# Performance work log

Measured on AMD Instinct MI355X. Metric: run time of the kernel, lower is better.

## Reference

```python
import jax, jax.numpy as jnp
import numpy as np

EMBED_DIM = 1024
NUM_HEADS = 16
HEAD_DIM = EMBED_DIM // NUM_HEADS


def setup_inputs() -> dict:
    key = jax.random.key(0)
    ks = jax.random.split(key, 5)
    B, T, C = 2, 2048, EMBED_DIM
    s_in = 1.0 / np.sqrt(C)
    x = jax.random.normal(ks[0], (B, T, C), dtype=jnp.float32)
    W_qkv = jax.random.normal(ks[1], (C, 3 * C), dtype=jnp.float32) * s_in
    b_qkv = jnp.zeros((3 * C,), dtype=jnp.float32)
    W_out = jax.random.normal(ks[2], (C, C), dtype=jnp.float32) * s_in
    b_out = jnp.zeros((C,), dtype=jnp.float32)
    return {"x": x, "W_qkv": W_qkv, "b_qkv": b_qkv, "W_out": W_out, "b_out": b_out}


def reference(x, W_qkv, b_qkv, W_out, b_out):
    B, T, C = x.shape
    H, D = NUM_HEADS, HEAD_DIM
    qkv = x @ W_qkv + b_qkv                      # [B,T,3C]
    qkv = qkv.reshape(B, T, 3, H, D)
    q = jnp.transpose(qkv[:, :, 0], (0, 2, 1, 3))  # [B,H,T,D]
    k = jnp.transpose(qkv[:, :, 1], (0, 2, 1, 3))
    v = jnp.transpose(qkv[:, :, 2], (0, 2, 1, 3))
    scores = jnp.einsum('bhtd,bhsd->bhts', q, k) / np.sqrt(D).astype(jnp.float32)
    attn = jax.nn.softmax(scores, axis=-1)
    ctx = jnp.einsum('bhts,bhsd->bhtd', attn, v)   # [B,H,T,D]
    ctx = jnp.transpose(ctx, (0, 2, 1, 3)).reshape(B, T, C)
    return ctx @ W_out + b_out
```

## Files before the change

kernel.cpp:

```cpp
#include <hip/hip_runtime.h>
#include <hip/hip_bf16.h>


typedef __attribute__((ext_vector_type(8)))  short short8;
typedef __attribute__((ext_vector_type(4)))  float floatx4;
typedef __attribute__((ext_vector_type(16))) float floatx16;

__device__ inline ushort f2bf(float f) {
    union { __hip_bfloat16 h; ushort u; } c; c.h = __float2bfloat16(f); return c.u;
}

__device__ inline uint cvt_pk_bf16(float a, float b) {
    uint r;
    asm("v_cvt_pk_bf16_f32 %0, %1, %2" : "=v"(r) : "v"(a), "v"(b));
    return r;
}

__device__ inline void gld16(const ushort* g, ushort* l) {
    __builtin_amdgcn_global_load_lds(
        (__attribute__((address_space(1))) void*)(g),
        (__attribute__((address_space(3))) void*)(l), 16, 0, 0);
}

__device__ inline void tile_transpose(const float* __restrict__ src, ushort* __restrict__ dst,
                                      int R, int C, int rt, int ct, int t, ushort* L)
{
    const int row = t >> 2, cc = (t & 3) * 16;
    const float* sp = src + (long)(rt * 64 + row) * C + ct * 64 + cc;
    ushort tmp[16];
    #pragma unroll
    for (int i = 0; i < 4; i++) {
        float4 v = *(const float4*)(sp + i * 4);
        tmp[i*4+0]=f2bf(v.x); tmp[i*4+1]=f2bf(v.y); tmp[i*4+2]=f2bf(v.z); tmp[i*4+3]=f2bf(v.w);
    }
    *(uint4*)&L[row * 72 + cc]     = *(uint4*)&tmp[0];
    *(uint4*)&L[row * 72 + cc + 8] = *(uint4*)&tmp[8];
    __syncthreads();
    const int c = t >> 2, rc = (t & 3) * 16;
    ushort o[16];
    #pragma unroll
    for (int j = 0; j < 16; j++) o[j] = L[(rc + j) * 72 + c];
    ushort* dp = dst + (long)(ct * 64 + c) * R + rt * 64 + rc;
    *(uint4*)dp       = *(uint4*)&o[0];
    *(uint4*)(dp + 8) = *(uint4*)&o[8];
}

__global__ __launch_bounds__(256) void prep_kernel(
    const float* __restrict__ x, const float* __restrict__ Wqkv, const float* __restrict__ Wout,
    ushort* __restrict__ xb, ushort* __restrict__ wqkvT, ushort* __restrict__ woutT)
{
    __shared__ __align__(16) ushort L[64 * 72];
    const int bid = blockIdx.x, t = threadIdx.x;
    if (bid < 2048) {
        long i = ((long)bid * 256 + t) * 8;
        float4 a = *(const float4*)(x + i);
        float4 b = *(const float4*)(x + i + 4);
        ushort tmp[8] = { f2bf(a.x), f2bf(a.y), f2bf(a.z), f2bf(a.w),
                          f2bf(b.x), f2bf(b.y), f2bf(b.z), f2bf(b.w) };
        *(uint4*)(xb + i) = *(uint4*)tmp;
    } else if (bid < 2048 + 768) {
        int idx = bid - 2048;
        tile_transpose(Wqkv, wqkvT, 1024, 3072, idx & 15, idx >> 4, t, L);
    } else {
        int idx = bid - 2048 - 768;
        tile_transpose(Wout, woutT, 1024, 1024, idx & 15, idx >> 4, t, L);
    }
}

#define QSCALE 0.18033688011112042f

__global__ __launch_bounds__(256, 3) void qkv_gemm_kernel(
    const ushort* __restrict__ A, const ushort* __restrict__ Bt,
    const float* __restrict__ bias,
    ushort* __restrict__ qbuf, ushort* __restrict__ kbuf, ushort* __restrict__ vtG)
{
    __shared__ __align__(16) ushort SMEM[16384];
    ushort* Asb[2] = { SMEM,        SMEM + 4096 };
    ushort* Bsb[2] = { SMEM + 8192, SMEM + 12288 };

    const int t = threadIdx.x;
    const int w = t >> 6, lane = t & 63;
    const int r = lane & 15, qq = lane >> 4;
    const int wm = w >> 1, wn = w & 1;

    const int id = blockIdx.x;
    const int xcd = id & 7, cidx = id >> 3;
    const int lx = cidx % 12, ly = cidx / 12;
    const int bx = (xcd & 1) * 12 + lx;
    const int by = (xcd >> 1) * 8 + ly;
    const int rowBase = by * 128, colBase = bx * 128;

    const int g_row = lane >> 2, g_kc = (lane & 3) * 8;
    const ushort* aP0 = A  + (long)(rowBase +      w * 16 + g_row) * 1024 + g_kc;
    const ushort* aP1 = A  + (long)(rowBase + 64 + w * 16 + g_row) * 1024 + g_kc;
    const ushort* bP0 = Bt + (long)(colBase +      w * 16 + g_row) * 1024 + g_kc;
    const ushort* bP1 = Bt + (long)(colBase + 64 + w * 16 + g_row) * 1024 + g_kc;

    floatx4 acc[4][4] = {};

    for (int k0 = 0; k0 < 1024; k0 += 64) {
        #pragma unroll
        for (int kk = 0; kk < 2; kk++) {
            gld16(aP0 + k0 + kk * 32, &Asb[kk][(w * 16) * 32]);
            gld16(aP1 + k0 + kk * 32, &Asb[kk][(64 + w * 16) * 32]);
            gld16(bP0 + k0 + kk * 32, &Bsb[kk][(w * 16) * 32]);
            gld16(bP1 + k0 + kk * 32, &Bsb[kk][(64 + w * 16) * 32]);
        }
        __syncthreads();
        #pragma unroll
        for (int kk = 0; kk < 2; kk++) {
            short8 af[4], bf4[4];
            #pragma unroll
            for (int tm = 0; tm < 4; tm++) af[tm]  = *(const short8*)&Asb[kk][(wm * 64 + tm * 16 + r) * 32 + qq * 8];
            #pragma unroll
            for (int tn = 0; tn < 4; tn++) bf4[tn] = *(const short8*)&Bsb[kk][(wn * 64 + tn * 16 + r) * 32 + qq * 8];
            #pragma unroll
            for (int tm = 0; tm < 4; tm++)
                #pragma unroll
                for (int tn = 0; tn < 4; tn++)
                    acc[tm][tn] = __builtin_amdgcn_mfma_f32_16x16x32_bf16(af[tm], bf4[tn], acc[tm][tn], 0, 0, 0);
        }
        __syncthreads();
    }

    if (colBase < 2048) {
        #pragma unroll
        for (int tn = 0; tn < 4; tn++) {
            int col = colBase + wn * 64 + tn * 16 + r;
            float bvv = bias[col];
            #pragma unroll
            for (int tm = 0; tm < 4; tm++) {
                #pragma unroll
                for (int reg = 0; reg < 4; reg++) {
                    int row = rowBase + wm * 64 + tm * 16 + qq * 4 + reg;
                    float val = acc[tm][tn][reg] + bvv;
                    if (colBase < 1024) qbuf[(long)row * 1024 + col]        = f2bf(val * QSCALE);
                    else                kbuf[(long)row * 1024 + col - 1024] = f2bf(val);
                }
            }
        }
    } else {
        ushort* L = SMEM;
        #pragma unroll
        for (int hh = 0; hh < 2; hh++) {
            __syncthreads();
            if (wn == hh) {
                #pragma unroll
                for (int tn = 0; tn < 4; tn++) {
                    int vc = tn * 16 + r;
                    float bvv = bias[colBase + wn * 64 + vc];
                    #pragma unroll
                    for (int tm = 0; tm < 4; tm++) {
                        int row0 = wm * 64 + tm * 16 + qq * 4;
                        ushort q4[4] = { f2bf(acc[tm][tn][0] + bvv), f2bf(acc[tm][tn][1] + bvv),
                                         f2bf(acc[tm][tn][2] + bvv), f2bf(acc[tm][tn][3] + bvv) };
                        *(uint2*)&L[vc * 136 + row0] = *(uint2*)q4;
                    }
                }
            }
            __syncthreads();
            int d = t >> 2, tq = (t & 3) * 32;
            int h_loc = ((colBase - 2048) >> 6) + hh;
            long vtrow = (long)((rowBase >> 11) * 16 + h_loc) * 64 + d;
            ushort* dst = vtG + vtrow * 2048 + (rowBase & 2047) + tq;
            #pragma unroll
            for (int i = 0; i < 4; i++)
                *(uint4*)(dst + 8 * i) = *(uint4*)&L[d * 136 + tq + 8 * i];
        }
    }
}

__global__ __launch_bounds__(256) void out_gemm_kernel(
    const ushort* __restrict__ A, const ushort* __restrict__ Bt,
    const float* __restrict__ bias, float* __restrict__ out)
{
    __shared__ __align__(16) ushort As[2][128 * 32];
    __shared__ __align__(16) ushort Bs[2][64 * 32];

    const int t = threadIdx.x;
    const int w = t >> 6, lane = t & 63;
    const int r = lane & 15, qq = lane >> 4;
    const int wm = w >> 1, wn = w & 1;

    const int id = blockIdx.x;
    const int xcd = id & 7, cidx = id >> 3;
    const int bx = (xcd & 1) * 8 + (cidx & 7);
    const int by = (xcd >> 1) * 8 + (cidx >> 3);
    const int rowBase = by * 128, colBase = bx * 64;

    const int g_row = lane >> 2, g_kc = (lane & 3) * 8;
    const ushort* aP0 = A  + (long)(rowBase +      w * 16 + g_row) * 1024 + g_kc;
    const ushort* aP1 = A  + (long)(rowBase + 64 + w * 16 + g_row) * 1024 + g_kc;
    const ushort* bP0 = Bt + (long)(colBase +      w * 16 + g_row) * 1024 + g_kc;

    floatx4 acc[4][2] = {};

    for (int k0 = 0; k0 < 1024; k0 += 64) {
        #pragma unroll
        for (int kk = 0; kk < 2; kk++) {
            gld16(aP0 + k0 + kk * 32, &As[kk][(w * 16) * 32]);
            gld16(aP1 + k0 + kk * 32, &As[kk][(64 + w * 16) * 32]);
            gld16(bP0 + k0 + kk * 32, &Bs[kk][(w * 16) * 32]);
        }
        __syncthreads();
        #pragma unroll
        for (int kk = 0; kk < 2; kk++) {
            short8 af[4], bf2[2];
            #pragma unroll
            for (int tm = 0; tm < 4; tm++) af[tm]  = *(const short8*)&As[kk][(wm * 64 + tm * 16 + r) * 32 + qq * 8];
            #pragma unroll
            for (int tn = 0; tn < 2; tn++) bf2[tn] = *(const short8*)&Bs[kk][(wn * 32 + tn * 16 + r) * 32 + qq * 8];
            #pragma unroll
            for (int tm = 0; tm < 4; tm++)
                #pragma unroll
                for (int tn = 0; tn < 2; tn++)
                    acc[tm][tn] = __builtin_amdgcn_mfma_f32_16x16x32_bf16(af[tm], bf2[tn], acc[tm][tn], 0, 0, 0);
        }
        __syncthreads();
    }

    #pragma unroll
    for (int tn = 0; tn < 2; tn++) {
        int col = colBase + wn * 32 + tn * 16 + r;
        float bvv = bias[col];
        #pragma unroll
        for (int tm = 0; tm < 4; tm++) {
            #pragma unroll
            for (int reg = 0; reg < 4; reg++) {
                int row = rowBase + wm * 64 + tm * 16 + qq * 4 + reg;
                out[(long)row * 1024 + col] = acc[tm][tn][reg] + bvv;
            }
        }
    }
}

__global__ __launch_bounds__(512, 4) void attn_kernel(
    ushort* __restrict__ qbuf, const ushort* __restrict__ kbuf,
    const ushort* __restrict__ vt)
{
    __shared__ __align__(16) ushort SM[2][2][2][64 * 72];

    const int t = threadIdx.x;
    const int w = t >> 6, lane = t & 63;
    const int m32 = lane & 31, hi = lane >> 5;
    const int h2 = w >> 2, wq = w & 3;

    const int id = blockIdx.x;
    const int j = id >> 3;
    const int bh = (id & 7) * 4 + (j >> 4);
    const int qt = j & 15;
    const int b = bh >> 4, h = bh & 15;
    const long qrow = (long)(b * 2048 + qt * 128 + wq * 32 + m32);

    short8 qfrag[4];
    #pragma unroll
    for (int dc = 0; dc < 4; dc++)
        qfrag[dc] = *(const short8*)(qbuf + qrow * 1024 + h * 64 + dc * 16 + hi * 8);

    short8 vones;
    #pragma unroll
    for (int i = 0; i < 8; i++) vones[i] = (short)0x3F80;

    const int ts = t & 255;
    const int srow = ts >> 2, scol = (ts & 3) * 16;
    const ushort* kP = kbuf + (long)(b * 2048 + h2 * 1024 + srow) * 1024 + h * 64 + scol;
    const ushort* vP = vt + (long)(bh * 64 + srow) * 2048 + h2 * 1024 + scol;

    floatx16 o[2] = {};
    floatx16 lacc = {};

    uint4 kr0, kr1, vr0, vr1;

    kr0 = *(const uint4*)kP;  kr1 = *(const uint4*)(kP + 8);
    vr0 = *(const uint4*)vP;  vr1 = *(const uint4*)(vP + 8);
    {
        ushort* Ks = SM[h2][0][0]; ushort* Vs = SM[h2][0][1];
        *(uint4*)&Ks[srow * 72 + scol]     = kr0;
        *(uint4*)&Ks[srow * 72 + scol + 8] = kr1;
        *(uint4*)&Vs[srow * 72 + scol]     = vr0;
        *(uint4*)&Vs[srow * 72 + scol + 8] = vr1;
    }
    kr0 = *(const uint4*)(kP + 64 * 1024); kr1 = *(const uint4*)(kP + 64 * 1024 + 8);
    vr0 = *(const uint4*)(vP + 64);        vr1 = *(const uint4*)(vP + 64 + 8);
    __syncthreads();

    #pragma unroll 2
    for (int tt = 0; tt < 16; tt++) {
        ushort* Ks = SM[h2][tt & 1][0];
        ushort* Vs = SM[h2][tt & 1][1];

        floatx16 s[2] = {};
        __builtin_amdgcn_s_setprio(1);
        #pragma unroll
        for (int c = 0; c < 2; c++) {
            #pragma unroll
            for (int dc = 0; dc < 4; dc++) {
                short8 kf = *(const short8*)&Ks[(c * 32 + m32) * 72 + dc * 16 + hi * 8];
                s[c] = __builtin_amdgcn_mfma_f32_32x32x16_bf16(kf, qfrag[dc], s[c], 0, 0, 0);
            }
        }
        __builtin_amdgcn_s_setprio(0);

        if (tt < 15) {
            ushort* Kn = SM[h2][(tt + 1) & 1][0];
            ushort* Vn = SM[h2][(tt + 1) & 1][1];
            *(uint4*)&Kn[srow * 72 + scol]     = kr0;
            *(uint4*)&Kn[srow * 72 + scol + 8] = kr1;
            *(uint4*)&Vn[srow * 72 + scol]     = vr0;
            *(uint4*)&Vn[srow * 72 + scol + 8] = vr1;
            if (tt < 14) {
                const ushort* kp = kP + (long)(tt + 2) * 64 * 1024;
                const ushort* vp = vP + (tt + 2) * 64;
                kr0 = *(const uint4*)kp; kr1 = *(const uint4*)(kp + 8);
                vr0 = *(const uint4*)vp; vr1 = *(const uint4*)(vp + 8);
            }
        }

        uint pk[2][8];
        #pragma unroll
        for (int c = 0; c < 2; c++) {
            #pragma unroll
            for (int i = 0; i < 8; i++) {
                float p0 = __builtin_amdgcn_exp2f(s[c][2 * i]);
                float p1 = __builtin_amdgcn_exp2f(s[c][2 * i + 1]);
                pk[c][i] = cvt_pk_bf16(p0, p1);
            }
        }

        __builtin_amdgcn_s_setprio(1);
        #pragma unroll
        for (int c = 0; c < 2; c++) {
            #pragma unroll
            for (int kc = 0; kc < 2; kc++) {
                uint a0 = pk[c][4 * kc + 0], b0 = pk[c][4 * kc + 2];
                asm("v_permlane32_swap_b32 %0, %1" : "+v"(a0), "+v"(b0));
                uint a1 = pk[c][4 * kc + 1], b1 = pk[c][4 * kc + 3];
                asm("v_permlane32_swap_b32 %0, %1" : "+v"(a1), "+v"(b1));
                union { uint u[4]; short8 s8; } cv;
                cv.u[0] = a0; cv.u[1] = a1; cv.u[2] = b0; cv.u[3] = b1;
                #pragma unroll
                for (int dt = 0; dt < 2; dt++) {
                    short8 vf = *(const short8*)&Vs[(dt * 32 + m32) * 72 + c * 32 + kc * 16 + hi * 8];
                    o[dt] = __builtin_amdgcn_mfma_f32_32x32x16_bf16(vf, cv.s8, o[dt], 0, 0, 0);
                }
                lacc = __builtin_amdgcn_mfma_f32_32x32x16_bf16(vones, cv.s8, lacc, 0, 0, 0);
            }
        }
        __builtin_amdgcn_s_setprio(0);

        __syncthreads();
    }

    float* OL = (float*)SM;
    float* LL = OL + 4 * 2048;
    if (h2 == 1) {
        #pragma unroll
        for (int dt = 0; dt < 2; dt++)
            #pragma unroll
            for (int i = 0; i < 16; i++)
                OL[wq * 2048 + (dt * 16 + i) * 64 + lane] = o[dt][i];
        LL[wq * 64 + lane] = lacc[0];
    }
    __syncthreads();
    if (h2 == 0) {
        float inv = 1.f / (lacc[0] + LL[wq * 64 + lane]);
        #pragma unroll
        for (int dt = 0; dt < 2; dt++) {
            #pragma unroll
            for (int i = 0; i < 16; i++) o[dt][i] += OL[wq * 2048 + (dt * 16 + i) * 64 + lane];
            #pragma unroll
            for (int g = 0; g < 4; g++) {
                ushort tmp[4] = { f2bf(o[dt][4*g+0] * inv), f2bf(o[dt][4*g+1] * inv),
                                  f2bf(o[dt][4*g+2] * inv), f2bf(o[dt][4*g+3] * inv) };
                *(uint2*)(qbuf + qrow * 1024 + h * 64 + dt * 32 + g * 8 + hi * 4) = *(uint2*)tmp;
            }
        }
    }
}

extern "C" void kernel_launch(void* const* d_in, const int* in_sizes, int n_in,
                              void* d_out, int out_size, void* d_ws, size_t ws_size,
                              hipStream_t stream) {
    const float* x     = (const float*)d_in[0];
    const float* W_qkv = (const float*)d_in[1];
    const float* b_qkv = (const float*)d_in[2];
    const float* W_out = (const float*)d_in[3];
    const float* b_out = (const float*)d_in[4];
    float* out = (float*)d_out;

    ushort* qbuf  = (ushort*)d_ws;
    ushort* kbuf  = qbuf + (size_t)4096 * 1024;
    ushort* vt    = kbuf + (size_t)4096 * 1024;
    ushort* woutT = vt + (size_t)2048 * 2048;
    ushort* wqkvT = woutT + (size_t)1024 * 1024;

    ushort* xb    = (ushort*)d_out;

    dim3 blk(256);
    prep_kernel<<<3072, blk, 0, stream>>>(x, W_qkv, W_out, xb, wqkvT, woutT);
    qkv_gemm_kernel<<<768, blk, 0, stream>>>(xb, wqkvT, b_qkv, qbuf, kbuf, vt);
    attn_kernel<<<512, dim3(512), 0, stream>>>(qbuf, kbuf, vt);
    out_gemm_kernel<<<512, blk, 0, stream>>>(qbuf, woutT, b_out, out);
}
```

Measured before the change: 186.8 us.

## Double-buffer LDS in QKV and output GEMMs to overlap loads with MFMA

Both projection GEMMs switch from a load-all-then-compute loop over 64-wide K steps to a ping-pong double buffer over 32-wide K steps. The next tile's global-to-LDS loads are issued before the current tile's MFMAs, and only one barrier is used per step. The goal is to hide global load latency behind matrix math. The cost is twice as many loop iterations and barriers, and it relies on the single barrier being enough to keep the buffers correctly ordered.

```diff
diff --git a/kernel.cpp b/kernel.cpp
--- a/kernel.cpp
+++ b/kernel.cpp
@@ -75,8 +75,6 @@
     ushort* __restrict__ qbuf, ushort* __restrict__ kbuf, ushort* __restrict__ vtG)
 {
     __shared__ __align__(16) ushort SMEM[16384];
-    ushort* Asb[2] = { SMEM,        SMEM + 4096 };
-    ushort* Bsb[2] = { SMEM + 8192, SMEM + 12288 };
 
     const int t = threadIdx.x;
     const int w = t >> 6, lane = t & 63;
@@ -90,36 +88,39 @@
     const int by = (xcd >> 1) * 8 + ly;
     const int rowBase = by * 128, colBase = bx * 128;
 
-    const int g_row = lane >> 2, g_kc = (lane & 3) * 8;
-    const ushort* aP0 = A  + (long)(rowBase +      w * 16 + g_row) * 1024 + g_kc;
-    const ushort* aP1 = A  + (long)(rowBase + 64 + w * 16 + g_row) * 1024 + g_kc;
-    const ushort* bP0 = Bt + (long)(colBase +      w * 16 + g_row) * 1024 + g_kc;
-    const ushort* bP1 = Bt + (long)(colBase + 64 + w * 16 + g_row) * 1024 + g_kc;
+    const int s_row = lane >> 2, s_k = (lane & 3) * 8;
+    const ushort* aS = A  + (long)(rowBase + w * 32 + s_row) * 1024 + s_k;
+    const ushort* bS = Bt + (long)(colBase + w * 32 + s_row) * 1024 + s_k;
 
     floatx4 acc[4][4] = {};
 
-    for (int k0 = 0; k0 < 1024; k0 += 64) {
-        #pragma unroll
-        for (int kk = 0; kk < 2; kk++) {
-            gld16(aP0 + k0 + kk * 32, &Asb[kk][(w * 16) * 32]);
-            gld16(aP1 + k0 + kk * 32, &Asb[kk][(64 + w * 16) * 32]);
-            gld16(bP0 + k0 + kk * 32, &Bsb[kk][(w * 16) * 32]);
-            gld16(bP1 + k0 + kk * 32, &Bsb[kk][(64 + w * 16) * 32]);
-        }
-        __syncthreads();
-        #pragma unroll
-        for (int kk = 0; kk < 2; kk++) {
-            short8 af[4], bf4[4];
-            #pragma unroll
-            for (int tm = 0; tm < 4; tm++) af[tm]  = *(const short8*)&Asb[kk][(wm * 64 + tm * 16 + r) * 32 + qq * 8];
-            #pragma unroll
-            for (int tn = 0; tn < 4; tn++) bf4[tn] = *(const short8*)&Bsb[kk][(wn * 64 + tn * 16 + r) * 32 + qq * 8];
-            #pragma unroll
-            for (int tm = 0; tm < 4; tm++)
-                #pragma unroll
-                for (int tn = 0; tn < 4; tn++)
-                    acc[tm][tn] = __builtin_amdgcn_mfma_f32_16x16x32_bf16(af[tm], bf4[tn], acc[tm][tn], 0, 0, 0);
-        }
+    gld16(aS,             SMEM + w * 1024);
+    gld16(aS + 16 * 1024, SMEM + w * 1024 + 512);
+    gld16(bS,             SMEM + 4096 + w * 1024);
+    gld16(bS + 16 * 1024, SMEM + 4096 + w * 1024 + 512);
+    __syncthreads();
+
+    #pragma unroll 2
+    for (int k = 0; k < 32; k++) {
+        ushort* cur = SMEM + (k & 1) * 8192;
+        if (k < 31) {
+            ushort* nxt = SMEM + ((k + 1) & 1) * 8192;
+            const int ko = (k + 1) * 32;
+            gld16(aS + ko,             nxt + w * 1024);
+            gld16(aS + ko + 16 * 1024, nxt + w * 1024 + 512);
+            gld16(bS + ko,             nxt + 4096 + w * 1024);
+            gld16(bS + ko + 16 * 1024, nxt + 4096 + w * 1024 + 512);
+        }
+        short8 af[4], bf4[4];
+        #pragma unroll
+        for (int tm = 0; tm < 4; tm++) af[tm]  = *(const short8*)&cur[(wm * 64 + tm * 16 + r) * 32 + qq * 8];
+        #pragma unroll
+        for (int tn = 0; tn < 4; tn++) bf4[tn] = *(const short8*)&cur[4096 + (wn * 64 + tn * 16 + r) * 32 + qq * 8];
+        #pragma unroll
+        for (int tm = 0; tm < 4; tm++)
+            #pragma unroll
+            for (int tn = 0; tn < 4; tn++)
+                acc[tm][tn] = __builtin_amdgcn_mfma_f32_16x16x32_bf16(af[tm], bf4[tn], acc[tm][tn], 0, 0, 0);
         __syncthreads();
     }
 
@@ -174,8 +175,7 @@
     const ushort* __restrict__ A, const ushort* __restrict__ Bt,
     const float* __restrict__ bias, float* __restrict__ out)
 {
-    __shared__ __align__(16) ushort As[2][128 * 32];
-    __shared__ __align__(16) ushort Bs[2][64 * 32];
+    __shared__ __align__(16) ushort SMEM[12288];
 
     const int t = threadIdx.x;
     const int w = t >> 6, lane = t & 63;
@@ -188,34 +188,37 @@
     const int by = (xcd >> 1) * 8 + (cidx >> 3);
     const int rowBase = by * 128, colBase = bx * 64;
 
-    const int g_row = lane >> 2, g_kc = (lane & 3) * 8;
-    const ushort* aP0 = A  + (long)(rowBase +      w * 16 + g_row) * 1024 + g_kc;
-    const ushort* aP1 = A  + (long)(rowBase + 64 + w * 16 + g_row) * 1024 + g_kc;
-    const ushort* bP0 = Bt + (long)(colBase +      w * 16 + g_row) * 1024 + g_kc;
+    const int s_row = lane >> 2, s_k = (lane & 3) * 8;
+    const ushort* aS = A  + (long)(rowBase + w * 32 + s_row) * 1024 + s_k;
+    const ushort* bS = Bt + (long)(colBase + w * 16 + s_row) * 1024 + s_k;
 
     floatx4 acc[4][2] = {};
 
-    for (int k0 = 0; k0 < 1024; k0 += 64) {
-        #pragma unroll
-        for (int kk = 0; kk < 2; kk++) {
-            gld16(aP0 + k0 + kk * 32, &As[kk][(w * 16) * 32]);
-            gld16(aP1 + k0 + kk * 32, &As[kk][(64 + w * 16) * 32]);
-            gld16(bP0 + k0 + kk * 32, &Bs[kk][(w * 16) * 32]);
-        }
-        __syncthreads();
-        #pragma unroll
-        for (int kk = 0; kk < 2; kk++) {
-            short8 af[4], bf2[2];
-            #pragma unroll
-            for (int tm = 0; tm < 4; tm++) af[tm]  = *(const short8*)&As[kk][(wm * 64 + tm * 16 + r) * 32 + qq * 8];
-            #pragma unroll
-            for (int tn = 0; tn < 2; tn++) bf2[tn] = *(const short8*)&Bs[kk][(wn * 32 + tn * 16 + r) * 32 + qq * 8];
-            #pragma unroll
-            for (int tm = 0; tm < 4; tm++)
-                #pragma unroll
-                for (int tn = 0; tn < 2; tn++)
-                    acc[tm][tn] = __builtin_amdgcn_mfma_f32_16x16x32_bf16(af[tm], bf2[tn], acc[tm][tn], 0, 0, 0);
-        }
+    gld16(aS,             SMEM + w * 1024);
+    gld16(aS + 16 * 1024, SMEM + w * 1024 + 512);
+    gld16(bS,             SMEM + 4096 + w * 512);
+    __syncthreads();
+
+    #pragma unroll 2
+    for (int k = 0; k < 32; k++) {
+        ushort* cur = SMEM + (k & 1) * 6144;
+        if (k < 31) {
+            ushort* nxt = SMEM + ((k + 1) & 1) * 6144;
+            const int ko = (k + 1) * 32;
+            gld16(aS + ko,             nxt + w * 1024);
+            gld16(aS + ko + 16 * 1024, nxt + w * 1024 + 512);
+            gld16(bS + ko,             nxt + 4096 + w * 512);
+        }
+        short8 af[4], bf2[2];
+        #pragma unroll
+        for (int tm = 0; tm < 4; tm++) af[tm]  = *(const short8*)&cur[(wm * 64 + tm * 16 + r) * 32 + qq * 8];
+        #pragma unroll
+        for (int tn = 0; tn < 2; tn++) bf2[tn] = *(const short8*)&cur[4096 + (wn * 32 + tn * 16 + r) * 32 + qq * 8];
+        #pragma unroll
+        for (int tm = 0; tm < 4; tm++)
+            #pragma unroll
+            for (int tn = 0; tn < 2; tn++)
+                acc[tm][tn] = __builtin_amdgcn_mfma_f32_16x16x32_bf16(af[tm], bf2[tn], acc[tm][tn], 0, 0, 0);
         __syncthreads();
     }
 
```

After: 187.2 us. No clear change (+0.2%).
